# Optimization experiments

Hardware: AMD Instinct MI355X
Metric: run time of the kernel (lower is better)

Reference implementation:

```python
import jax, jax.numpy as jnp
import numpy as np

V = 25; NE = 5; DIM = 192; H = 6; HD = 32; N = 64; T = 64
SCALE = HD ** -0.5
COEFF = 0.4
NTU_EDGES = [(1,2),(2,21),(3,21),(4,3),(5,21),(6,5),(7,6),(8,7),(9,21),(10,9),(11,10),(12,11),(13,1),(14,13),(15,14),(16,15),(17,1),(18,17),(19,18),(20,19),(22,23),(23,8),(24,25),(25,12)]

def _compute_hops():
    # replicate MHSA.__init__ hop-distance computation (A = [I, adj, adj] summed+binarized)
    adj = np.zeros((V, V))
    for i, j in NTU_EDGES:
        adj[i-1, j-1] = 1.0; adj[j-1, i-1] = 1.0
    h1 = ((np.eye(V) + adj) != 0).astype(np.float64)
    h = [None] * V
    h[0] = np.eye(V); h[1] = h1
    hops = np.zeros((V, V))
    for i in range(2, V):
        h[i] = ((h[i-1] @ h1.T) != 0).astype(np.float64)
    for i in range(V-1, 0, -1):
        if np.any(h[i] - h[i-1]):
            h[i] = h[i] - h[i-1]
            hops += i * h[i]
    return hops.astype(np.int32)

def setup_inputs() -> dict:
    key = jax.random.key(0)
    ks = jax.random.split(key, 12)
    hops = jnp.asarray(_compute_hops())
    n_hop = int(hops.max()) + 1
    std = 0.02
    return {
        "x": jax.random.normal(ks[0], (N, DIM, T, V), jnp.float32),
        "joint_label": jnp.arange(V, dtype=jnp.int32) % NE,  # all 5 hyperedge labels present
        "groups": NE,  # unused by forward (kept for signature fidelity)
        "he_weight": jax.random.uniform(ks[1], (NE,), jnp.float32),
        "hops": hops,
        "ln_g": jnp.ones((DIM,), jnp.float32),
        "ln_b": jnp.zeros((DIM,), jnp.float32),
        "hgc_w": std * jax.random.normal(ks[2], (DIM, DIM), jnp.float32),
        "q_w": std * jax.random.normal(ks[3], (DIM, DIM), jnp.float32),
        "kv_w": std * jax.random.normal(ks[4], (2 * DIM, DIM), jnp.float32),
        "proj_w": std * jax.random.normal(ks[5], (DIM, HD), jnp.float32),  # grouped 1x1 conv, groups=6
        "proj_b": jnp.zeros((DIM,), jnp.float32),
        "rpe": std * jax.random.normal(ks[6], (n_hop, DIM), jnp.float32),
        "w1": std * jax.random.normal(ks[7], (H, HD), jnp.float32),
        "outer": jnp.tile(jnp.eye(V, dtype=jnp.float32), (H, 1, 1)) + std * jax.random.normal(ks[8], (H, V, V), jnp.float32),
        "alpha": 0.1 * jnp.ones((1,), jnp.float32),
        "lin1_w": std * jax.random.normal(ks[9], (T // 5, T), jnp.float32),
        "lin1_b": jnp.zeros((T // 5,), jnp.float32),
        "lin2_w": std * jax.random.normal(ks[10], (T, T // 5), jnp.float32),
        "lin2_b": jnp.zeros((T,), jnp.float32),
    }

def _forward(x, joint_label, he_weight, hops, ln_g, ln_b, hgc_w, q_w, kv_w, proj_w, proj_b, rpe, w1, outer, alpha, lin1_w, lin1_b, lin2_w, lin2_b):
    N_, C, T_, V_ = x.shape
    # ---- HGattn branch: hypergraph conv + temporal squeeze-excite gate ----
    label = jax.nn.one_hot(joint_label, NE, dtype=x.dtype)            # (V, 5)
    label1 = label / label.sum(0, keepdims=True)
    label1 = label1 / jnp.sqrt(label.sum(1, keepdims=True))
    label1 = (he_weight[None, :] * label1).T                          # (5, V)
    norm_label = label / label.sum(1, keepdims=True)
    h_adj = norm_label @ label1                                       # (V, V)
    z = jnp.einsum('nctv,vw->nctw', x, h_adj)
    op = jnp.einsum('nctv,oc->notv', z, hgc_w)                        # (N, dim, T, V) 1x1 conv
    op_tr = op.transpose(0, 1, 3, 2)                                  # (N, dim, V, T)
    s = op_tr.mean(axis=(1, 2))                                       # (N, T) global avg pool over (dim, V)
    g = jax.nn.sigmoid(jax.nn.relu(s @ lin1_w.T + lin1_b) @ lin2_w.T + lin2_b)  # (N, T)
    op_final = op_tr + COEFF * (op_tr * g[:, None, None, :])
    e = op_final.transpose(0, 1, 3, 2)                                # (N, dim, T, V)
    # ---- LayerNorm over channel dim ----
    xc = x.transpose(0, 2, 3, 1)                                      # (N, T, V, C)
    mu = xc.mean(-1, keepdims=True)
    var = xc.var(-1, keepdims=True)
    xn = (((xc - mu) / jnp.sqrt(var + 1e-5)) * ln_g + ln_b).transpose(0, 3, 1, 2)
    # ---- MHSA with hop-indexed relative bias, e-branch scores, outer fusion ----
    q = jnp.einsum('nctv,oc->notv', xn, q_w).reshape(N_, H, HD, T_, V_).transpose(0, 3, 1, 4, 2)   # (N,T,H,V,hd)
    kv = jnp.einsum('nctv,oc->notv', xn, kv_w).reshape(N_, 2, H, HD, T_, V_)
    k = kv[:, 0].transpose(0, 3, 1, 4, 2)
    v = kv[:, 1].transpose(0, 3, 1, 4, 2)
    e_k = e.reshape(N_, H, HD, T_, V_).transpose(0, 3, 1, 4, 2)
    k_r = rpe[hops].reshape(V_, V_, H, HD)                            # hop-distance relative position table
    b = jnp.einsum('bthnc,nmhc->bthnm', q, k_r)
    c = jnp.einsum('bthnc,bthmc->bthnm', q, e_k)
    d = jnp.einsum('hc,bthmc->bthm', w1, e_k)[..., None, :]
    a = jnp.einsum('bthnc,bthmc->bthnm', q, k)
    attn = jax.nn.softmax((a + b + c + d) * SCALE, axis=-1)
    o = jnp.einsum('bthnm,bthmc->bthnc', alpha * attn + outer[None, None], v)
    o = o.transpose(0, 1, 2, 4, 3).reshape(N_, T_, DIM, V_).transpose(0, 2, 1, 3)  # (N, dim, T, V)
    # grouped 1x1 conv projection (groups = H)
    og = o.reshape(N_, H, HD, T_, V_)
    wg = proj_w.reshape(H, HD, HD)
    o = jnp.einsum('ngitv,goi->ngotv', og, wg).reshape(N_, DIM, T_, V_) + proj_b[None, :, None, None]
    return x + o  # dim_in == dim -> identity skip

def reference(x, joint_label, groups, he_weight, hops, ln_g, ln_b, hgc_w, q_w, kv_w, proj_w, proj_b, rpe, w1, outer, alpha, lin1_w, lin1_b, lin2_w, lin2_b):
    return _forward(x, joint_label, he_weight, hops, ln_g, ln_b, hgc_w, q_w, kv_w, proj_w, proj_b, rpe, w1, outer, alpha, lin1_w, lin1_b, lin2_w, lin2_b)
```

## Files before the change

### kernel.cpp

```cpp
#include <hip/hip_runtime.h>
#include <hip/hip_bf16.h>

using bf16 = __hip_bfloat16;
typedef __bf16 bf16x8 __attribute__((ext_vector_type(8)));
typedef float f32x4 __attribute__((ext_vector_type(4)));

constexpr int kDim = 192;
constexpr int kH = 6;
constexpr int kHd = 32;
constexpr int kN = 64;
constexpr int kT = 64;
constexpr int kV = 25;
constexpr int kP = kT * kV;
constexpr int kNCstride = kDim * kP;
constexpr float kScale = 0.17677669529663687f;
constexpr float kCoeff = 0.4f;

__global__ void __launch_bounds__(256) setup_kernel(
    const int* __restrict__ jl, const float* __restrict__ hew,
    const float* __restrict__ hgc, const float* __restrict__ qw,
    const float* __restrict__ kvw, const float* __restrict__ rpe,
    const float* __restrict__ proj_w, const float* __restrict__ lng,
    const float* __restrict__ lnb, int n_hop, float* __restrict__ hadj,
    bf16* __restrict__ Wb, float* __restrict__ G, float* __restrict__ Bb,
    bf16* __restrict__ RPEb, bf16* __restrict__ pwb) {
  const int bid = blockIdx.x;
  const int tid = threadIdx.x;
  if (bid < 576) {
    int i = bid * 256 + tid;
    float v;
    if (i < 36864) {
      v = hgc[i];
    } else {
      int local = i - 36864;
      int c = local % kDim;
      v = (local < 36864) ? qw[local] : kvw[local - 36864];
      v *= lng[c];
    }
    Wb[i] = __float2bfloat16(v);
  } else if (bid == 576) {
    __shared__ int lbl[kV];
    __shared__ int cnt[8];
    if (tid < 8) cnt[tid] = 0;
    __syncthreads();
    if (tid < kV) { lbl[tid] = jl[tid]; atomicAdd(&cnt[lbl[tid]], 1); }
    __syncthreads();
    for (int idx = tid; idx < kV * kV; idx += 256) {
      int v = idx / kV, w = idx - v * kV;
      float val = 0.f;
      if (lbl[v] == lbl[w]) val = hew[lbl[v]] / (float)cnt[lbl[v]];
      hadj[idx] = val;
    }
  } else if (bid == 577) {
    for (int i = tid; i < kH * 16 * kHd; i += 256) {
      int h = i >> 9, hp = (i >> 5) & 15, d = i & 31;
      float v = (hp < n_hop) ? rpe[hp * kDim + h * kHd + d] : 0.f;
      RPEb[i] = __float2bfloat16(v);
    }
    for (int i = tid; i < kDim * kHd; i += 256)
      pwb[i] = __float2bfloat16(proj_w[i]);
  } else {
    int o = (bid - 578) * 4 + (tid >> 6);
    int lane = tid & 63;
    const float* Wr =
        (o < kDim) ? (qw + (size_t)o * kDim) : (kvw + (size_t)(o - kDim) * kDim);
    float gs = 0.f, bs = 0.f;
    for (int c = lane; c < kDim; c += 64) {
      float wv = Wr[c];
      gs += wv * lng[c];
      bs += wv * lnb[c];
    }
    for (int off = 32; off > 0; off >>= 1) {
      gs += __shfl_down(gs, off);
      bs += __shfl_down(bs, off);
    }
    if (lane == 0) { G[o] = gs; Bb[o] = bs; }
  }
}

__global__ void __launch_bounds__(256) prep_kernel(
    const float* __restrict__ x, bf16* __restrict__ XR, float* __restrict__ mu,
    float* __restrict__ rstd) {
  __shared__ float ps[kV][25], ps2[kV][25];
  const int tid = threadIdx.x;
  const int t = blockIdx.x, n = blockIdx.y;
  const float* xb = x + (size_t)n * kNCstride + t * kV;
  size_t ob = ((size_t)n * kP + t * kV) * kDim;
  for (int idx = tid; idx < 600; idx += 256) {
    int p = idx % 25, c8 = idx / 25;
    float a = 0.f, b = 0.f;
    union { uint4 u; __bf16 h[8]; } pk;
#pragma unroll
    for (int i = 0; i < 8; ++i) {
      float v = xb[(size_t)(c8 * 8 + i) * kP + p];
      a += v;
      b += v * v;
      pk.h[i] = (__bf16)v;
    }
    *reinterpret_cast<uint4*>(XR + ob + (size_t)p * kDim + c8 * 8) = pk.u;
    ps[p][c8] = a;
    ps2[p][c8] = b;
  }
  __syncthreads();
  if (tid < kV) {
    float a = 0.f, b = 0.f;
#pragma unroll
    for (int c8 = 0; c8 < 24; ++c8) { a += ps[tid][c8]; b += ps2[tid][c8]; }
    float m = a * (1.f / kDim);
    float var = b * (1.f / kDim) - m * m;
    int gid = n * kP + t * kV + tid;
    mu[gid] = m;
    rstd[gid] = rsqrtf(var + 1e-5f);
  }
}

__global__ void __launch_bounds__(64) mfma_gemm_kernel(
    const bf16* __restrict__ A, const bf16* __restrict__ B,
    bf16* __restrict__ out) {
  int id = blockIdx.x;
  int per = gridDim.x >> 3;
  int wg = (id & 7) * per + (id >> 3);
  int n = wg / (25 * 3);
  int rem = wg - n * (25 * 3);
  const int pb = (rem / 3) * 64;
  const int ob = (rem % 3) * 64;
  const int l = threadIdx.x;
  B += (size_t)n * kNCstride;
  out += (size_t)n * kP * kDim;
  f32x4 acc[4][4] = {};
  const int lm = l & 15;
  const int lk = (l >> 4) * 8;
  for (int kb = 0; kb < kDim; kb += 32) {
    bf16x8 af[4], bfv[4];
#pragma unroll
    for (int mf = 0; mf < 4; ++mf)
      af[mf] = *reinterpret_cast<const bf16x8*>(
          A + (size_t)(ob + mf * 16 + lm) * kDim + kb + lk);
#pragma unroll
    for (int nf = 0; nf < 4; ++nf)
      bfv[nf] = *reinterpret_cast<const bf16x8*>(
          B + (size_t)(pb + nf * 16 + lm) * kDim + kb + lk);
#pragma unroll
    for (int mf = 0; mf < 4; ++mf)
#pragma unroll
      for (int nf = 0; nf < 4; ++nf)
        acc[mf][nf] = __builtin_amdgcn_mfma_f32_16x16x32_bf16(
            af[mf], bfv[nf], acc[mf][nf], 0, 0, 0);
  }
  const int r0 = (l >> 4) * 4;
#pragma unroll
  for (int mf = 0; mf < 4; ++mf) {
    const int o0 = ob + mf * 16 + r0;
#pragma unroll
    for (int nf = 0; nf < 4; ++nf) {
      const int p = pb + nf * 16 + lm;
      union { uint2 u; bf16 b[4]; } pk;
#pragma unroll
      for (int r = 0; r < 4; ++r) pk.b[r] = __float2bfloat16(acc[mf][nf][r]);
      *reinterpret_cast<uint2*>(out + (size_t)p * kDim + o0) = pk.u;
    }
  }
}

__global__ void __launch_bounds__(64) gemm_qkv_kernel(
    const bf16* __restrict__ A, const bf16* __restrict__ B,
    bf16* __restrict__ QK, bf16* __restrict__ VT,
    const float* __restrict__ muA, const float* __restrict__ rsA,
    const float* __restrict__ G, const float* __restrict__ Bb) {
  __shared__ ushort vt_s[64 * 52];
  int id = blockIdx.x;
  int per = gridDim.x >> 3;
  int wg = (id & 7) * per + (id >> 3);
  int n = wg / 288;
  int rem = wg - n * 288;
  const int pt = rem / 9;
  const int ob = rem % 9;
  const int pb = pt * 50;
  const int l = threadIdx.x;
  B += (size_t)n * kNCstride;
  f32x4 acc[4][4] = {};
  const int lm = l & 15;
  const int lk = (l >> 4) * 8;
  for (int kb = 0; kb < kDim; kb += 32) {
    bf16x8 af[4], bfv[4];
#pragma unroll
    for (int mf = 0; mf < 4; ++mf)
      af[mf] = *reinterpret_cast<const bf16x8*>(
          A + (size_t)(ob * 64 + mf * 16 + lm) * kDim + kb + lk);
#pragma unroll
    for (int nf = 0; nf < 4; ++nf)
      bfv[nf] = *reinterpret_cast<const bf16x8*>(
          B + (size_t)(pb + nf * 16 + lm) * kDim + kb + lk);
#pragma unroll
    for (int mf = 0; mf < 4; ++mf)
#pragma unroll
      for (int nf = 0; nf < 4; ++nf)
        acc[mf][nf] = __builtin_amdgcn_mfma_f32_16x16x32_bf16(
            af[mf], bfv[nf], acc[mf][nf], 0, 0, 0);
  }
  const int r0 = (l >> 4) * 4;
  float rsv[4], muv[4];
#pragma unroll
  for (int nf = 0; nf < 4; ++nf) {
    int pidx = n * kP + min(pb + nf * 16 + lm, kP - 1);
    rsv[nf] = rsA[pidx];
    muv[nf] = muA[pidx];
  }
  if (ob < 6) {
    QK += (size_t)n * kP * 384;
#pragma unroll
    for (int mf = 0; mf < 4; ++mf) {
      const int o0 = ob * 64 + mf * 16 + r0;
      float4 g4 = *reinterpret_cast<const float4*>(G + o0);
      float4 b4 = *reinterpret_cast<const float4*>(Bb + o0);
      float ga[4] = {g4.x, g4.y, g4.z, g4.w};
      float ba[4] = {b4.x, b4.y, b4.z, b4.w};
#pragma unroll
      for (int nf = 0; nf < 4; ++nf) {
        int pl = nf * 16 + lm;
        if (pl < 50) {
          union { uint2 u; bf16 b[4]; } pk;
#pragma unroll
          for (int r = 0; r < 4; ++r)
            pk.b[r] = __float2bfloat16(
                rsv[nf] * (acc[mf][nf][r] - muv[nf] * ga[r]) + ba[r]);
          *reinterpret_cast<uint2*>(QK + (size_t)(pb + pl) * 384 + o0) = pk.u;
        }
      }
    }
  } else {
    const int d0 = (ob - 6) * 64;
    bf16* vt_b = reinterpret_cast<bf16*>(vt_s);
#pragma unroll
    for (int mf = 0; mf < 4; ++mf) {
      const int o0 = 384 + d0 + mf * 16 + r0;
      float4 g4 = *reinterpret_cast<const float4*>(G + o0);
      float4 b4 = *reinterpret_cast<const float4*>(Bb + o0);
      float ga[4] = {g4.x, g4.y, g4.z, g4.w};
      float ba[4] = {b4.x, b4.y, b4.z, b4.w};
#pragma unroll
      for (int nf = 0; nf < 4; ++nf) {
        int pl = nf * 16 + lm;
        if (pl < 50) {
#pragma unroll
          for (int r = 0; r < 4; ++r)
            vt_b[(mf * 16 + r0 + r) * 52 + pl] = __float2bfloat16(
                rsv[nf] * (acc[mf][nf][r] - muv[nf] * ga[r]) + ba[r]);
        }
      }
    }
#pragma unroll
    for (int it = 0; it < 16; ++it) {
      int rowi = it * 8 + (l >> 3);
      int tsel = rowi >> 6, olocal = rowi & 63;
      int vcol = (l & 7) * 4;
      union { uint2 u; ushort s[4]; } pk;
#pragma unroll
      for (int q = 0; q < 4; ++q) {
        int v = vcol + q;
        pk.s[q] = (v < kV) ? vt_s[olocal * 52 + tsel * 25 + v] : (ushort)0;
      }
      size_t addr =
          ((size_t)(n * kT + pt * 2 + tsel) * kDim + d0 + olocal) * 32 + vcol;
      *reinterpret_cast<uint2*>(VT + addr) = pk.u;
    }
  }
}

__global__ void __launch_bounds__(256) haapply_kernel(
    bf16* __restrict__ OP, const float* __restrict__ hadjg,
    float* __restrict__ s_out) {
  __shared__ ushort tile[kV * kDim];
  __shared__ float ha[640];
  __shared__ float red[4];
  const int tid = threadIdx.x;
  const int t = blockIdx.x, n = blockIdx.y;
  size_t base = ((size_t)n * kP + t * kV) * kDim;
  for (int i = tid; i < kV * kV; i += 256) ha[i] = hadjg[i];
  const uint2* src = reinterpret_cast<const uint2*>(OP + base);
  uint2* dst2 = reinterpret_cast<uint2*>(tile);
  for (int i = tid; i < kV * kDim / 4; i += 256) dst2[i] = src[i];
  __syncthreads();
  float ssum = 0.f;
  for (int idx = tid; idx < 600; idx += 256) {
    int c8 = idx % 24, w = idx / 24;
    float acc[8] = {0.f, 0.f, 0.f, 0.f, 0.f, 0.f, 0.f, 0.f};
    for (int v = 0; v < kV; ++v) {
      float coef = ha[v * kV + w];
      union { uint4 u; __bf16 h[8]; } ld;
      ld.u = *reinterpret_cast<const uint4*>(tile + v * kDim + c8 * 8);
#pragma unroll
      for (int j = 0; j < 8; ++j) acc[j] += coef * (float)ld.h[j];
    }
    union { uint4 u; __bf16 h[8]; } pk;
    float s8 = 0.f;
#pragma unroll
    for (int j = 0; j < 8; ++j) { pk.h[j] = (__bf16)acc[j]; s8 += acc[j]; }
    *reinterpret_cast<uint4*>(OP + base + (size_t)w * kDim + c8 * 8) = pk.u;
    ssum += s8;
  }
  for (int off = 32; off > 0; off >>= 1) ssum += __shfl_down(ssum, off);
  if ((tid & 63) == 0) red[tid >> 6] = ssum;
  __syncthreads();
  if (tid == 0)
    s_out[n * kT + t] = (red[0] + red[1] + red[2] + red[3]) *
                        (1.f / (float)(kDim * kV));
}

__global__ void gate_kernel(const float* __restrict__ s,
                            const float* __restrict__ w1l,
                            const float* __restrict__ b1,
                            const float* __restrict__ w2l,
                            const float* __restrict__ b2,
                            float* __restrict__ gatef) {
  __shared__ float sh[kT];
  __shared__ float hid[12];
  int n = blockIdx.x, t = threadIdx.x;
  sh[t] = s[n * kT + t];
  __syncthreads();
  if (t < 12) {
    float a = b1[t];
    for (int j = 0; j < kT; ++j) a += sh[j] * w1l[t * kT + j];
    hid[t] = fmaxf(a, 0.f);
  }
  __syncthreads();
  float a = b2[t];
  for (int j = 0; j < 12; ++j) a += hid[j] * w2l[t * 12 + j];
  float g = 1.f / (1.f + __expf(-a));
  gatef[n * kT + t] = 1.f + kCoeff * g;
}

__global__ void __launch_bounds__(384) attn_kernel(
    const bf16* __restrict__ QK, const bf16* __restrict__ VT,
    const bf16* __restrict__ OP, const float* __restrict__ gatef,
    const int* __restrict__ hops, const bf16* __restrict__ RPEb,
    const float* __restrict__ w1, const float* __restrict__ outer,
    const float* __restrict__ alpha_p, const bf16* __restrict__ pwb,
    const float* __restrict__ proj_b, const float* __restrict__ x,
    float* __restrict__ out) {
  __shared__ ushort wls[kH][1280];
  __shared__ unsigned char hopsB[kV][32];
  const int tid = threadIdx.x;
  const int lane = tid & 63;
  const int h = tid >> 6;
  const int t = blockIdx.x, n = blockIdx.y;
  const int nt = n * kT + t;
  const int lm = lane & 15, g = lane >> 4;
  const bool w1ok = (lm + 16) < kV;

  const bf16* Qbase = QK + (size_t)(nt * kV) * 384;
  const bf16* Ebase = OP + (size_t)(nt * kV) * kDim;
  const int colO = h * kHd + g * 8;
  bf16x8 qf[2], kf[2], ef[2];
#pragma unroll
  for (int mf = 0; mf < 2; ++mf) {
    const bf16* row = Qbase + (size_t)(mf * 16 + lm) * 384;
    qf[mf] = *reinterpret_cast<const bf16x8*>(row + colO);
    kf[mf] = *reinterpret_cast<const bf16x8*>(row + kDim + colO);
    ef[mf] = *reinterpret_cast<const bf16x8*>(
        Ebase + (size_t)(mf * 16 + lm) * kDim + colO);
  }
  bf16x8 rf = *reinterpret_cast<const bf16x8*>(RPEb + (h * 16 + lm) * kHd + g * 8);
  bf16x8 vb[2], pwf[2];
#pragma unroll
  for (int nf = 0; nf < 2; ++nf) {
    vb[nf] = *reinterpret_cast<const bf16x8*>(
        VT + ((size_t)(nt * kDim + h * kHd + nf * 16 + lm)) * 32 + g * 8);
    pwf[nf] = *reinterpret_cast<const bf16x8*>(
        pwb + (h * kHd + nf * 16 + lm) * kHd + g * 8);
  }
  float w1v[8];
  {
    float4 wa = *reinterpret_cast<const float4*>(w1 + h * kHd + g * 8);
    float4 wb = *reinterpret_cast<const float4*>(w1 + h * kHd + g * 8 + 4);
    w1v[0] = wa.x; w1v[1] = wa.y; w1v[2] = wa.z; w1v[3] = wa.w;
    w1v[4] = wb.x; w1v[5] = wb.y; w1v[6] = wb.z; w1v[7] = wb.w;
  }
  float outv0[8], outv1[8];
#pragma unroll
  for (int mf = 0; mf < 2; ++mf)
#pragma unroll
    for (int r = 0; r < 4; ++r) {
      int v = mf * 16 + g * 4 + r;
      int vc = v < kV ? v : kV - 1;
      const float* orow = outer + h * (kV * kV) + vc * kV;
      outv0[mf * 4 + r] = orow[lm];
      outv1[mf * 4 + r] = w1ok ? orow[lm + 16] : 0.f;
    }
  const float f = gatef[nt];
  const float alpha = alpha_p[0];

  for (int i = tid; i < kV * 32; i += 384) {
    int v = i >> 5, w = i & 31;
    hopsB[v][w] = (w < kV) ? (unsigned char)hops[v * kV + w] : 0;
  }
  __syncthreads();
  bf16* Pp = (bf16*)&wls[h][0];

  float dt[2];
#pragma unroll
  for (int nf = 0; nf < 2; ++nf) {
    float a = 0.f;
#pragma unroll
    for (int j = 0; j < 8; ++j) a += w1v[j] * (float)ef[nf][j];
    a += __shfl_xor(a, 16);
    a += __shfl_xor(a, 32);
    dt[nf] = f * a;
  }
  bf16x8 kef[2];
#pragma unroll
  for (int nf = 0; nf < 2; ++nf)
#pragma unroll
    for (int j = 0; j < 8; ++j)
      kef[nf][j] = (__bf16)((float)kf[nf][j] + f * (float)ef[nf][j]);

  f32x4 aS[2][2] = {};
  f32x4 aR[2] = {};
#pragma unroll
  for (int mf = 0; mf < 2; ++mf) {
#pragma unroll
    for (int nf = 0; nf < 2; ++nf)
      aS[mf][nf] = __builtin_amdgcn_mfma_f32_16x16x32_bf16(qf[mf], kef[nf],
                                                           aS[mf][nf], 0, 0, 0);
    aR[mf] = __builtin_amdgcn_mfma_f32_16x16x32_bf16(qf[mf], rf, aR[mf], 0, 0, 0);
  }

#pragma unroll
  for (int mf = 0; mf < 2; ++mf) {
#pragma unroll
    for (int r = 0; r < 4; ++r) {
      int v = mf * 16 + g * 4 + r;
      int vc = v < kV ? v : kV - 1;
      int hp0 = hopsB[vc][lm];
      int hp1 = hopsB[vc][lm + 16];
      float qr0 = __shfl(aR[mf][r], g * 16 + hp0);
      float qr1 = __shfl(aR[mf][r], g * 16 + hp1);
      float s0 = (aS[mf][0][r] + qr0 + dt[0]) * kScale;
      float s1 = (aS[mf][1][r] + qr1 + dt[1]) * kScale;
      if (!w1ok) s1 = -3.0e38f;
      float m = fmaxf(s0, s1);
#pragma unroll
      for (int d = 1; d < 16; d <<= 1) m = fmaxf(m, __shfl_xor(m, d));
      float e0 = __expf(s0 - m);
      float e1 = w1ok ? __expf(s1 - m) : 0.f;
      float sum = e0 + e1;
#pragma unroll
      for (int d = 1; d < 16; d <<= 1) sum += __shfl_xor(sum, d);
      float inv = alpha / sum;
      Pp[v * 40 + lm] = __float2bfloat16(e0 * inv + outv0[mf * 4 + r]);
      Pp[v * 40 + lm + 16] =
          __float2bfloat16(w1ok ? e1 * inv + outv1[mf * 4 + r] : 0.f);
    }
  }

  bf16x8 pa[2];
#pragma unroll
  for (int mf = 0; mf < 2; ++mf)
    pa[mf] = *reinterpret_cast<const bf16x8*>(Pp + (mf * 16 + lm) * 40 + g * 8);
  f32x4 aO[2][2] = {};
#pragma unroll
  for (int mf = 0; mf < 2; ++mf)
#pragma unroll
    for (int nf = 0; nf < 2; ++nf)
      aO[mf][nf] =
          __builtin_amdgcn_mfma_f32_16x16x32_bf16(pa[mf], vb[nf], aO[mf][nf], 0, 0, 0);

#pragma unroll
  for (int mf = 0; mf < 2; ++mf)
#pragma unroll
    for (int nf = 0; nf < 2; ++nf)
#pragma unroll
      for (int r = 0; r < 4; ++r)
        Pp[(mf * 16 + g * 4 + r) * 40 + nf * 16 + lm] =
            __float2bfloat16(aO[mf][nf][r]);
  bf16x8 oa[2];
#pragma unroll
  for (int nf = 0; nf < 2; ++nf)
    oa[nf] = *reinterpret_cast<const bf16x8*>(Pp + (nf * 16 + lm) * 40 + g * 8);
  f32x4 aF[2][2] = {};
#pragma unroll
  for (int mf = 0; mf < 2; ++mf)
#pragma unroll
    for (int nf = 0; nf < 2; ++nf)
      aF[mf][nf] =
          __builtin_amdgcn_mfma_f32_16x16x32_bf16(pwf[mf], oa[nf], aF[mf][nf], 0, 0, 0);

#pragma unroll
  for (int mf = 0; mf < 2; ++mf) {
#pragma unroll
    for (int r = 0; r < 4; ++r) {
      int oo = mf * 16 + g * 4 + r;
      int c = h * kHd + oo;
      float pbv = proj_b[c];
      size_t gbase = (size_t)n * kNCstride + (size_t)c * kP + t * kV;
#pragma unroll
      for (int nf = 0; nf < 2; ++nf) {
        int v = nf * 16 + lm;
        if (v < kV) out[gbase + v] = x[gbase + v] + aF[mf][nf][r] + pbv;
      }
    }
  }
}

extern "C" void kernel_launch(void* const* d_in, const int* in_sizes, int n_in,
                              void* d_out, int out_size, void* d_ws,
                              size_t ws_size, hipStream_t stream) {
  const float* x = (const float*)d_in[0];
  const int* joint_label = (const int*)d_in[1];
  const float* he_weight = (const float*)d_in[3];
  const int* hops = (const int*)d_in[4];
  const float* ln_g = (const float*)d_in[5];
  const float* ln_b = (const float*)d_in[6];
  const float* hgc_w = (const float*)d_in[7];
  const float* q_w = (const float*)d_in[8];
  const float* kv_w = (const float*)d_in[9];
  const float* proj_w = (const float*)d_in[10];
  const float* proj_b = (const float*)d_in[11];
  const float* rpe = (const float*)d_in[12];
  const float* w1 = (const float*)d_in[13];
  const float* outer = (const float*)d_in[14];
  const float* alpha = (const float*)d_in[15];
  const float* lin1_w = (const float*)d_in[16];
  const float* lin1_b = (const float*)d_in[17];
  const float* lin2_w = (const float*)d_in[18];
  const float* lin2_b = (const float*)d_in[19];
  const int n_hop = in_sizes[12] / kDim;

  char* w = (char*)d_ws;
  bf16* QK = (bf16*)w;
  w += (size_t)kN * kP * 2 * kDim * 2;
  bf16* XR = (bf16*)w;
  w += (size_t)kN * kP * kDim * 2;
  bf16* OP = (bf16*)w;
  w += (size_t)kN * kP * kDim * 2;
  w += 65536;
  bf16* VT = (bf16*)w;
  w += (size_t)kN * kT * kDim * 32 * 2;
  bf16* Wb = (bf16*)w;
  w += (size_t)768 * kDim * 2;
  bf16* RPEb = (bf16*)w;
  w += (size_t)kH * 16 * kHd * 2;
  bf16* pwb = (bf16*)w;
  w += (size_t)kDim * kHd * 2;
  float* hadj = (float*)w;
  w += 1024 * 4;
  float* s_ws = (float*)w;
  w += kN * kT * 4;
  float* gatef = (float*)w;
  w += kN * kT * 4;
  float* mu = (float*)w;
  w += (size_t)kN * kP * 4;
  float* rstd = (float*)w;
  w += (size_t)kN * kP * 4;
  float* G = (float*)w;
  w += 576 * 4;
  float* Bb = (float*)w;
  w += 576 * 4;

  hipLaunchKernelGGL(setup_kernel, dim3(722), dim3(256), 0, stream,
                     joint_label, he_weight, hgc_w, q_w, kv_w, rpe, proj_w,
                     ln_g, ln_b, n_hop, hadj, Wb, G, Bb, RPEb, pwb);
  hipLaunchKernelGGL(prep_kernel, dim3(kT, kN), dim3(256), 0, stream, x, XR,
                     mu, rstd);
  hipLaunchKernelGGL(mfma_gemm_kernel, dim3(25 * 3 * kN), dim3(64), 0, stream,
                     Wb, XR, OP);
  hipLaunchKernelGGL(haapply_kernel, dim3(kT, kN), dim3(256), 0, stream, OP,
                     hadj, s_ws);
  hipLaunchKernelGGL(gate_kernel, dim3(kN), dim3(kT), 0, stream, s_ws, lin1_w,
                     lin1_b, lin2_w, lin2_b, gatef);
  hipLaunchKernelGGL(gemm_qkv_kernel, dim3(32 * 9 * kN), dim3(64), 0, stream,
                     Wb + (size_t)192 * kDim, XR, QK, VT, mu, rstd, G, Bb);
  hipLaunchKernelGGL(attn_kernel, dim3(kT, kN), dim3(384), 0, stream, QK, VT,
                     OP, gatef, hops, RPEb, w1, outer, alpha, pwb, proj_b, x,
                     (float*)d_out);
}
```

Baseline: 374.1 us.

## Fuse hypergraph adjacency apply into HGC GEMM and split attention per head

```diff
diff --git a/kernel.cpp b/kernel.cpp
--- a/kernel.cpp
+++ b/kernel.cpp
@@ -15,6 +15,12 @@
 constexpr int kNCstride = kDim * kP;
 constexpr float kScale = 0.17677669529663687f;
 constexpr float kCoeff = 0.4f;
+
+__device__ __forceinline__ ushort bf16bits(float v) {
+  union { ushort s; bf16 b; } cv;
+  cv.b = __float2bfloat16(v);
+  return cv.s;
+}
 
 __global__ void __launch_bounds__(256) setup_kernel(
     const int* __restrict__ jl, const float* __restrict__ hew,
@@ -114,19 +120,23 @@
   }
 }
 
-__global__ void __launch_bounds__(64) mfma_gemm_kernel(
+__global__ void __launch_bounds__(64) hgc_kernel(
     const bf16* __restrict__ A, const bf16* __restrict__ B,
-    bf16* __restrict__ out) {
+    bf16* __restrict__ OP, const float* __restrict__ hadjg,
+    float* __restrict__ part) {
+  __shared__ ushort tile[64 * 52];
+  __shared__ float ha[640];
   int id = blockIdx.x;
   int per = gridDim.x >> 3;
   int wg = (id & 7) * per + (id >> 3);
-  int n = wg / (25 * 3);
-  int rem = wg - n * (25 * 3);
-  const int pb = (rem / 3) * 64;
-  const int ob = (rem % 3) * 64;
+  int n = wg / 96;
+  int rem = wg - n * 96;
+  const int pt = rem / 3;
+  const int ob = rem % 3;
+  const int pb = pt * 50;
   const int l = threadIdx.x;
+  for (int i = l; i < kV * kV; i += 64) ha[i] = hadjg[i];
   B += (size_t)n * kNCstride;
-  out += (size_t)n * kP * kDim;
   f32x4 acc[4][4] = {};
   const int lm = l & 15;
   const int lk = (l >> 4) * 8;
@@ -135,7 +145,7 @@
 #pragma unroll
     for (int mf = 0; mf < 4; ++mf)
       af[mf] = *reinterpret_cast<const bf16x8*>(
-          A + (size_t)(ob + mf * 16 + lm) * kDim + kb + lk);
+          A + (size_t)(ob * 64 + mf * 16 + lm) * kDim + kb + lk);
 #pragma unroll
     for (int nf = 0; nf < 4; ++nf)
       bfv[nf] = *reinterpret_cast<const bf16x8*>(
@@ -149,16 +159,60 @@
   }
   const int r0 = (l >> 4) * 4;
 #pragma unroll
-  for (int mf = 0; mf < 4; ++mf) {
-    const int o0 = ob + mf * 16 + r0;
+  for (int mf = 0; mf < 4; ++mf)
 #pragma unroll
     for (int nf = 0; nf < 4; ++nf) {
-      const int p = pb + nf * 16 + lm;
-      union { uint2 u; bf16 b[4]; } pk;
-#pragma unroll
-      for (int r = 0; r < 4; ++r) pk.b[r] = __float2bfloat16(acc[mf][nf][r]);
-      *reinterpret_cast<uint2*>(out + (size_t)p * kDim + o0) = pk.u;
-    }
+      int pl = nf * 16 + lm;
+      if (pl < 50) {
+#pragma unroll
+        for (int r = 0; r < 4; ++r)
+          tile[(mf * 16 + r0 + r) * 52 + pl] = bf16bits(acc[mf][nf][r]);
+      }
+    }
+  __syncthreads();
+  float row[50];
+#pragma unroll
+  for (int j = 0; j < 12; ++j) {
+    union { uint2 u; ushort s[4]; } ld;
+    ld.u = *reinterpret_cast<const uint2*>(tile + l * 52 + j * 4);
+#pragma unroll
+    for (int q = 0; q < 4; ++q) {
+      union { ushort s; bf16 b; } cv;
+      cv.s = ld.s[q];
+      row[j * 4 + q] = __bfloat162float(cv.b);
+    }
+  }
+  {
+    union { uint u; ushort s[2]; } ld;
+    ld.u = *reinterpret_cast<const uint*>(tile + l * 52 + 48);
+#pragma unroll
+    for (int q = 0; q < 2; ++q) {
+      union { ushort s; bf16 b; } cv;
+      cv.s = ld.s[q];
+      row[48 + q] = __bfloat162float(cv.b);
+    }
+  }
+  float ss[2] = {0.f, 0.f};
+#pragma unroll
+  for (int tsel = 0; tsel < 2; ++tsel) {
+    size_t obase = ((size_t)n * kP + (pt * 2 + tsel) * 25) * kDim + ob * 64 + l;
+#pragma unroll
+    for (int w = 0; w < kV; ++w) {
+      float a = 0.f;
+#pragma unroll
+      for (int v = 0; v < kV; ++v) a += row[tsel * 25 + v] * ha[v * kV + w];
+      OP[obase + (size_t)w * kDim] = __float2bfloat16(a);
+      ss[tsel] += a;
+    }
+  }
+#pragma unroll
+  for (int off = 32; off > 0; off >>= 1) {
+    ss[0] += __shfl_down(ss[0], off);
+    ss[1] += __shfl_down(ss[1], off);
+  }
+  if (l == 0) {
+    part[(n * kT + pt * 2) * 4 + ob] = ss[0];
+    part[(n * kT + pt * 2 + 1) * 4 + ob] = ss[1];
   }
 }
 
@@ -230,7 +284,6 @@
     }
   } else {
     const int d0 = (ob - 6) * 64;
-    bf16* vt_b = reinterpret_cast<bf16*>(vt_s);
 #pragma unroll
     for (int mf = 0; mf < 4; ++mf) {
       const int o0 = 384 + d0 + mf * 16 + r0;
@@ -244,11 +297,12 @@
         if (pl < 50) {
 #pragma unroll
           for (int r = 0; r < 4; ++r)
-            vt_b[(mf * 16 + r0 + r) * 52 + pl] = __float2bfloat16(
+            vt_s[(mf * 16 + r0 + r) * 52 + pl] = bf16bits(
                 rsv[nf] * (acc[mf][nf][r] - muv[nf] * ga[r]) + ba[r]);
         }
       }
     }
+    __syncthreads();
 #pragma unroll
     for (int it = 0; it < 16; ++it) {
       int rowi = it * 8 + (l >> 3);
@@ -267,47 +321,7 @@
   }
 }
 
-__global__ void __launch_bounds__(256) haapply_kernel(
-    bf16* __restrict__ OP, const float* __restrict__ hadjg,
-    float* __restrict__ s_out) {
-  __shared__ ushort tile[kV * kDim];
-  __shared__ float ha[640];
-  __shared__ float red[4];
-  const int tid = threadIdx.x;
-  const int t = blockIdx.x, n = blockIdx.y;
-  size_t base = ((size_t)n * kP + t * kV) * kDim;
-  for (int i = tid; i < kV * kV; i += 256) ha[i] = hadjg[i];
-  const uint2* src = reinterpret_cast<const uint2*>(OP + base);
-  uint2* dst2 = reinterpret_cast<uint2*>(tile);
-  for (int i = tid; i < kV * kDim / 4; i += 256) dst2[i] = src[i];
-  __syncthreads();
-  float ssum = 0.f;
-  for (int idx = tid; idx < 600; idx += 256) {
-    int c8 = idx % 24, w = idx / 24;
-    float acc[8] = {0.f, 0.f, 0.f, 0.f, 0.f, 0.f, 0.f, 0.f};
-    for (int v = 0; v < kV; ++v) {
-      float coef = ha[v * kV + w];
-      union { uint4 u; __bf16 h[8]; } ld;
-      ld.u = *reinterpret_cast<const uint4*>(tile + v * kDim + c8 * 8);
-#pragma unroll
-      for (int j = 0; j < 8; ++j) acc[j] += coef * (float)ld.h[j];
-    }
-    union { uint4 u; __bf16 h[8]; } pk;
-    float s8 = 0.f;
-#pragma unroll
-    for (int j = 0; j < 8; ++j) { pk.h[j] = (__bf16)acc[j]; s8 += acc[j]; }
-    *reinterpret_cast<uint4*>(OP + base + (size_t)w * kDim + c8 * 8) = pk.u;
-    ssum += s8;
-  }
-  for (int off = 32; off > 0; off >>= 1) ssum += __shfl_down(ssum, off);
-  if ((tid & 63) == 0) red[tid >> 6] = ssum;
-  __syncthreads();
-  if (tid == 0)
-    s_out[n * kT + t] = (red[0] + red[1] + red[2] + red[3]) *
-                        (1.f / (float)(kDim * kV));
-}
-
-__global__ void gate_kernel(const float* __restrict__ s,
+__global__ void gate_kernel(const float* __restrict__ part,
                             const float* __restrict__ w1l,
                             const float* __restrict__ b1,
                             const float* __restrict__ w2l,
@@ -316,7 +330,9 @@
   __shared__ float sh[kT];
   __shared__ float hid[12];
   int n = blockIdx.x, t = threadIdx.x;
-  sh[t] = s[n * kT + t];
+  int nt = n * kT + t;
+  sh[t] = (part[nt * 4] + part[nt * 4 + 1] + part[nt * 4 + 2]) *
+          (1.f / (float)(kDim * kV));
   __syncthreads();
   if (t < 12) {
     float a = b1[t];
@@ -327,10 +343,10 @@
   float a = b2[t];
   for (int j = 0; j < 12; ++j) a += hid[j] * w2l[t * 12 + j];
   float g = 1.f / (1.f + __expf(-a));
-  gatef[n * kT + t] = 1.f + kCoeff * g;
-}
-
-__global__ void __launch_bounds__(384) attn_kernel(
+  gatef[nt] = 1.f + kCoeff * g;
+}
+
+__global__ void __launch_bounds__(64) attn_kernel(
     const bf16* __restrict__ QK, const bf16* __restrict__ VT,
     const bf16* __restrict__ OP, const float* __restrict__ gatef,
     const int* __restrict__ hops, const bf16* __restrict__ RPEb,
@@ -338,12 +354,12 @@
     const float* __restrict__ alpha_p, const bf16* __restrict__ pwb,
     const float* __restrict__ proj_b, const float* __restrict__ x,
     float* __restrict__ out) {
-  __shared__ ushort wls[kH][1280];
-  __shared__ unsigned char hopsB[kV][32];
-  const int tid = threadIdx.x;
-  const int lane = tid & 63;
-  const int h = tid >> 6;
-  const int t = blockIdx.x, n = blockIdx.y;
+  __shared__ ushort wls[1280];
+  const int lane = threadIdx.x;
+  const int bx = blockIdx.x;
+  const int h = bx % kH;
+  const int t = bx / kH;
+  const int n = blockIdx.y;
   const int nt = n * kT + t;
   const int lm = lane & 15, g = lane >> 4;
   const bool w1ok = (lm + 16) < kV;
@@ -369,40 +385,16 @@
     pwf[nf] = *reinterpret_cast<const bf16x8*>(
         pwb + (h * kHd + nf * 16 + lm) * kHd + g * 8);
   }
-  float w1v[8];
-  {
-    float4 wa = *reinterpret_cast<const float4*>(w1 + h * kHd + g * 8);
-    float4 wb = *reinterpret_cast<const float4*>(w1 + h * kHd + g * 8 + 4);
-    w1v[0] = wa.x; w1v[1] = wa.y; w1v[2] = wa.z; w1v[3] = wa.w;
-    w1v[4] = wb.x; w1v[5] = wb.y; w1v[6] = wb.z; w1v[7] = wb.w;
-  }
-  float outv0[8], outv1[8];
-#pragma unroll
-  for (int mf = 0; mf < 2; ++mf)
-#pragma unroll
-    for (int r = 0; r < 4; ++r) {
-      int v = mf * 16 + g * 4 + r;
-      int vc = v < kV ? v : kV - 1;
-      const float* orow = outer + h * (kV * kV) + vc * kV;
-      outv0[mf * 4 + r] = orow[lm];
-      outv1[mf * 4 + r] = w1ok ? orow[lm + 16] : 0.f;
-    }
   const float f = gatef[nt];
   const float alpha = alpha_p[0];
 
-  for (int i = tid; i < kV * 32; i += 384) {
-    int v = i >> 5, w = i & 31;
-    hopsB[v][w] = (w < kV) ? (unsigned char)hops[v * kV + w] : 0;
-  }
-  __syncthreads();
-  bf16* Pp = (bf16*)&wls[h][0];
-
   float dt[2];
 #pragma unroll
   for (int nf = 0; nf < 2; ++nf) {
     float a = 0.f;
 #pragma unroll
-    for (int j = 0; j < 8; ++j) a += w1v[j] * (float)ef[nf][j];
+    for (int j = 0; j < 8; ++j)
+      a += w1[h * kHd + g * 8 + j] * (float)ef[nf][j];
     a += __shfl_xor(a, 16);
     a += __shfl_xor(a, 32);
     dt[nf] = f * a;
@@ -425,14 +417,15 @@
     aR[mf] = __builtin_amdgcn_mfma_f32_16x16x32_bf16(qf[mf], rf, aR[mf], 0, 0, 0);
   }
 
+  bf16* Pp = (bf16*)&wls[0];
 #pragma unroll
   for (int mf = 0; mf < 2; ++mf) {
 #pragma unroll
     for (int r = 0; r < 4; ++r) {
       int v = mf * 16 + g * 4 + r;
       int vc = v < kV ? v : kV - 1;
-      int hp0 = hopsB[vc][lm];
-      int hp1 = hopsB[vc][lm + 16];
+      int hp0 = hops[vc * kV + lm];
+      int hp1 = w1ok ? hops[vc * kV + lm + 16] : 0;
       float qr0 = __shfl(aR[mf][r], g * 16 + hp0);
       float qr1 = __shfl(aR[mf][r], g * 16 + hp1);
       float s0 = (aS[mf][0][r] + qr0 + dt[0]) * kScale;
@@ -447,9 +440,10 @@
 #pragma unroll
       for (int d = 1; d < 16; d <<= 1) sum += __shfl_xor(sum, d);
       float inv = alpha / sum;
-      Pp[v * 40 + lm] = __float2bfloat16(e0 * inv + outv0[mf * 4 + r]);
+      const float* orow = outer + h * (kV * kV) + vc * kV;
+      Pp[v * 40 + lm] = __float2bfloat16(e0 * inv + orow[lm]);
       Pp[v * 40 + lm + 16] =
-          __float2bfloat16(w1ok ? e1 * inv + outv1[mf * 4 + r] : 0.f);
+          __float2bfloat16(w1ok ? e1 * inv + orow[lm + 16] : 0.f);
     }
   }
 
@@ -544,8 +538,8 @@
   w += (size_t)kDim * kHd * 2;
   float* hadj = (float*)w;
   w += 1024 * 4;
-  float* s_ws = (float*)w;
-  w += kN * kT * 4;
+  float* part = (float*)w;
+  w += (size_t)kN * kT * 4 * 4;
   float* gatef = (float*)w;
   w += kN * kT * 4;
   float* mu = (float*)w;
@@ -562,15 +556,13 @@
                      ln_g, ln_b, n_hop, hadj, Wb, G, Bb, RPEb, pwb);
   hipLaunchKernelGGL(prep_kernel, dim3(kT, kN), dim3(256), 0, stream, x, XR,
                      mu, rstd);
-  hipLaunchKernelGGL(mfma_gemm_kernel, dim3(25 * 3 * kN), dim3(64), 0, stream,
-                     Wb, XR, OP);
-  hipLaunchKernelGGL(haapply_kernel, dim3(kT, kN), dim3(256), 0, stream, OP,
-                     hadj, s_ws);
-  hipLaunchKernelGGL(gate_kernel, dim3(kN), dim3(kT), 0, stream, s_ws, lin1_w,
+  hipLaunchKernelGGL(hgc_kernel, dim3(96 * kN), dim3(64), 0, stream, Wb, XR,
+                     OP, hadj, part);
+  hipLaunchKernelGGL(gate_kernel, dim3(kN), dim3(kT), 0, stream, part, lin1_w,
                      lin1_b, lin2_w, lin2_b, gatef);
   hipLaunchKernelGGL(gemm_qkv_kernel, dim3(32 * 9 * kN), dim3(64), 0, stream,
                      Wb + (size_t)192 * kDim, XR, QK, VT, mu, rstd, G, Bb);
-  hipLaunchKernelGGL(attn_kernel, dim3(kT, kN), dim3(384), 0, stream, QK, VT,
-                     OP, gatef, hops, RPEb, w1, outer, alpha, pwb, proj_b, x,
-                     (float*)d_out);
-}
+  hipLaunchKernelGGL(attn_kernel, dim3(kT * kH, kN), dim3(64), 0, stream, QK,
+                     VT, OP, gatef, hops, RPEb, w1, outer, alpha, pwb, proj_b,
+                     x, (float*)d_out);
+}
```

Measured after the change: 424.3 us. 13.4% more time.
